# Kernel tuning notes

Hardware: AMD Instinct MI355X
Metric: run time of the kernel (lower is better)

Reference implementation:

```python
import jax, jax.numpy as jnp
import numpy as np

B, NC, NL, E, H = 64, 32, 64, 256, 256
CCLIP = 10.0


def _norm(x):
    # eps avoids NaN grads when two sampled nodes coincide
    return jnp.sqrt(jnp.sum(x * x, axis=-1) + 1e-12)


def setup_inputs() -> dict:
    key = jax.random.key(0)
    ks = jax.random.split(key, 24)
    s = 0.05
    inp = {
        "node_context": jax.random.normal(ks[0], (B, NC, NL, E), jnp.float32),
        "cell_context": jax.random.normal(ks[1], (B, NC, E), jnp.float32),
        "original_data": jax.random.uniform(ks[2], (B, NC, NL, 2), jnp.float32),
        "high_mask": jnp.zeros((B, NC), jnp.int32),
        "low_mask": jnp.zeros((B, NC, NL), jnp.int32),
        # high decoder params
        "init_w": jax.random.uniform(ks[3], (2 * E,), jnp.float32, -1.0, 1.0),
        "Wc": jax.random.normal(ks[4], (E, E), jnp.float32) * s,
        "bc": jnp.zeros((E,), jnp.float32),
        "Wv": jax.random.normal(ks[5], (2 * E, E), jnp.float32) * s,
        "bv": jnp.zeros((E,), jnp.float32),
        "hWq": jax.random.normal(ks[6], (E, H), jnp.float32) * s,
        "hbq": jnp.zeros((H,), jnp.float32),
        "hWr": jax.random.normal(ks[7], (E, H), jnp.float32) * s,
        "hbr": jnp.zeros((H,), jnp.float32),
        "hv": jax.random.normal(ks[8], (H,), jnp.float32) * s,
        # low decoder params
        "low_init_w": jax.random.uniform(ks[9], (2 * E,), jnp.float32, -1.0, 1.0),
        "lWc": jax.random.normal(ks[10], (E, E), jnp.float32) * s,
        "lbc": jnp.zeros((E,), jnp.float32),
        "lWv": jax.random.normal(ks[11], (2 * E, E), jnp.float32) * s,
        "lbv": jnp.zeros((E,), jnp.float32),
        "lWq": jax.random.normal(ks[12], (E, H), jnp.float32) * s,
        "lbq": jnp.zeros((H,), jnp.float32),
        "lWr": jax.random.normal(ks[13], (E, H), jnp.float32) * s,
        "lbr": jnp.zeros((H,), jnp.float32),
        "lv": jax.random.normal(ks[14], (H,), jnp.float32) * s,
    }
    return inp


def reference(node_context, cell_context, original_data, high_mask, low_mask,
              init_w, Wc, bc, Wv, bv, hWq, hbq, hWr, hbr, hv,
              low_init_w, lWc, lbc, lWv, lbv, lWq, lbq, lWr, lbr, lv):
    B_, NC_, NL_, E_ = node_context.shape
    aB = jnp.arange(B_)

    def pointer_logits(query, target, mask, Wq, bq, Wr, br, v):
        # query [B,E], target [B,S,E], mask [B,S] (1 = visited/blocked)
        q = query @ Wq + bq                                  # [B,H]
        r = jnp.einsum('bse,eh->bsh', target, Wr) + br       # [B,S,H]
        u = jnp.tanh(q[:, None, :] + r) @ v                  # [B,S]
        u = CCLIP * jnp.tanh(u)
        return jnp.where(mask > 0, -1e9, u)

    def low_decode(ctx, coords, mask, key):
        # ctx [B,NL,E], coords [B,NL,2], mask [B,NL]
        h_bar = jnp.mean(ctx, axis=1) @ lWc + lbc
        query = h_bar + (low_init_w @ lWv + lbv)
        keys = jax.random.split(key, NL_)

        def sample(query, mask, k):
            logits = pointer_logits(query, ctx, mask, lWq, lbq, lWr, lbr, lv)
            idx = jax.random.categorical(k, logits)
            logp = jnp.take_along_axis(jax.nn.log_softmax(logits), idx[:, None], axis=1)[:, 0]
            return idx, logp, mask.at[aB, idx].set(1)

        idx0, logp0, mask = sample(query, mask, keys[0])
        init_h = ctx[aB, idx0]                                # first selected node embedding
        query = h_bar + (jnp.concatenate([init_h, init_h], -1) @ lWv + lbv)
        init_node = coords[:, 0]                              # tour starts at local node 0
        rew0 = _norm(coords[aB, idx0] - init_node)

        def step(carry, k):
            query, mask, cur = carry
            idx, logp, mask = sample(query, mask, k)
            h = ctx[aB, idx]
            query = h_bar + (jnp.concatenate([init_h, h], -1) @ lWv + lbv)
            rew = _norm(coords[aB, idx] - coords[aB, cur])
            return (query, mask, idx), (logp, rew)

        (_, _, last_idx), (logps, rews) = jax.lax.scan(step, (query, mask, idx0), keys[1:])
        return logp0 + logps.sum(0), rew0 + rews.sum(0), init_node, coords[aB, last_idx]

    h_bar = jnp.mean(cell_context, axis=1) @ Wc + bc
    query = h_bar + (init_w @ Wv + bv)
    hkeys = jax.random.split(jax.random.key(42), NC_)
    lkeys = jax.random.split(jax.random.key(7), NC_)

    def sample_high(query, hmask, k):
        logits = pointer_logits(query, cell_context, hmask, hWq, hbq, hWr, hbr, hv)
        idx = jax.random.categorical(k, logits)
        logp = jnp.take_along_axis(jax.nn.log_softmax(logits), idx[:, None], axis=1)[:, 0]
        return idx, logp, hmask.at[aB, idx].set(1)

    def run_cell(idx, k_lo, last_node):
        llogp, lR, init_node, new_last = low_decode(
            node_context[aB, idx], original_data[aB, idx], low_mask[aB, idx], k_lo)
        return llogp, lR + _norm(init_node - last_node), new_last

    # high step 0 (sets init_h)
    idx0, hlogp0, hmask = sample_high(query, high_mask, hkeys[0])
    init_h = cell_context[aB, idx0]
    query = h_bar + (jnp.concatenate([init_h, init_h], -1) @ Wv + bv)
    llogp0, rew0, last_node = run_cell(idx0, lkeys[0], jnp.zeros((B_, 2), node_context.dtype))

    def high_step(carry, ks):
        query, hmask, last_node = carry
        k_hi, k_lo = ks
        idx, hlogp, hmask = sample_high(query, hmask, k_hi)
        h = cell_context[aB, idx]
        query = h_bar + (jnp.concatenate([init_h, h], -1) @ Wv + bv)
        llogp, rew, last_node = run_cell(idx, k_lo, last_node)
        return (query, hmask, last_node), (hlogp + llogp, rew)

    _, (logps, rews) = jax.lax.scan(high_step, (query, hmask, last_node), (hkeys[1:], lkeys[1:]))
    total_log_prob = hlogp0 + llogp0 + logps.sum(0)   # [B]
    total_reward = rew0 + rews.sum(0)                 # [B]
    return total_log_prob, total_reward
```

## Files before the change

kernel.cpp:

```cpp
#include <hip/hip_runtime.h>
#include <cstdint>
#include <cstddef>

#define B_  64
#define NC_ 32
#define NL_ 64
#define E_  256
#define H_  256

__device__ __forceinline__ void tf2x32(unsigned k0, unsigned k1,
                                       unsigned c0, unsigned c1,
                                       unsigned &o0, unsigned &o1) {
  unsigned ks2 = k0 ^ k1 ^ 0x1BD11BDAu;
  unsigned x0 = c0 + k0, x1 = c1 + k1;
#define TFR(r) { x0 += x1; x1 = (x1 << r) | (x1 >> (32 - r)); x1 ^= x0; }
  TFR(13) TFR(15) TFR(26) TFR(6)   x0 += k1;  x1 += ks2 + 1u;
  TFR(17) TFR(29) TFR(16) TFR(24)  x0 += ks2; x1 += k0 + 2u;
  TFR(13) TFR(15) TFR(26) TFR(6)   x0 += k0;  x1 += k1 + 3u;
  TFR(17) TFR(29) TFR(16) TFR(24)  x0 += k1;  x1 += ks2 + 4u;
  TFR(13) TFR(15) TFR(26) TFR(6)   x0 += ks2; x1 += k0 + 5u;
#undef TFR
  o0 = x0; o1 = x1;
}

__device__ __forceinline__ float gumbel_bits(unsigned k0, unsigned k1, unsigned flat) {
  unsigned a, b;
  tf2x32(k0, k1, 0u, flat, a, b);
  unsigned bits = a ^ b;
  float f = __uint_as_float(0x3F800000u | (bits >> 9)) - 1.0f;
  f = fmaxf(f, 1.17549435e-38f);
  return -logf(-logf(f));
}

__device__ __forceinline__ float ftanh(float x) {
  float e = __expf(2.0f * x);
  return fmaf(-2.0f, __builtin_amdgcn_rcpf(e + 1.0f), 1.0f);
}

__global__ __launch_bounds__(256) void k0_kernel(
    const float* __restrict__ init_w, const float* __restrict__ Wv,
    const float* __restrict__ hWq,
    const float* __restrict__ low_init_w, const float* __restrict__ lWv,
    const float* __restrict__ lWq, const float* __restrict__ lvin,
    unsigned* __restrict__ hkeys, unsigned* __restrict__ lkeys,
    float* __restrict__ g0h, float* __restrict__ g0l,
    float* __restrict__ Lsum) {
  int tid = threadIdx.x;
  __shared__ float s_iwv[E_], s_liwv[E_];
  if (tid < 32) {
    unsigned a, b;
    tf2x32(0u, 42u, 0u, (unsigned)tid, a, b);
    hkeys[2*tid] = a; hkeys[2*tid+1] = b;
    tf2x32(0u, 7u, 0u, (unsigned)tid, a, b);
    lkeys[2*tid] = a; lkeys[2*tid+1] = b;
  }
  if (tid == 0) {
    float s = 0.f;
    for (int k = 0; k < 256; ++k) s += lvin[k];
    Lsum[0] = s;
  }
  {
    float a = 0.f, a2 = 0.f;
    for (int k = 0; k < 2*E_; ++k) {
      a  = fmaf(init_w[k],     Wv[(size_t)k*E_ + tid], a);
      a2 = fmaf(low_init_w[k], lWv[(size_t)k*E_ + tid], a2);
    }
    s_iwv[tid] = a; s_liwv[tid] = a2;
  }
  __syncthreads();
  {
    float a = 0.f, a2 = 0.f;
    for (int e = 0; e < E_; ++e) {
      a  = fmaf(s_iwv[e],  hWq[(size_t)e*H_ + tid], a);
      a2 = fmaf(s_liwv[e], lWq[(size_t)e*H_ + tid], a2);
    }
    g0h[tid] = a; g0l[tid] = a2;
  }
}

__global__ __launch_bounds__(256) void k_mean(const float* __restrict__ in,
                                              float* __restrict__ out, int G) {
  int row = blockIdx.x, h = threadIdx.x;
  const float* p = in + (size_t)row * G * E_ + h;
  float a = 0.f;
  for (int g = 0; g < G; ++g) a += p[(size_t)g * E_];
  out[(size_t)row * E_ + h] = a * (1.0f / G);
}

__global__ __launch_bounds__(256) void k_gemm(
    const float* __restrict__ A, int lda, const float* __restrict__ avec,
    const float* __restrict__ W, const float* __restrict__ bias,
    float* __restrict__ C, int M, int N, int K) {
  __shared__ float As[16][17];
  int i0 = blockIdx.x * 16, j0 = blockIdx.y * 64;
  int tx = threadIdx.x & 63, ty = threadIdx.x >> 6;
  int j = j0 + tx;
  float acc[4] = {0.f, 0.f, 0.f, 0.f};
  for (int kk = 0; kk < K; kk += 16) {
    int r = threadIdx.x >> 4, cc = threadIdx.x & 15;
    float av = A[(size_t)(i0 + r) * lda + kk + cc];
    if (avec) av += avec[kk + cc];
    As[r][cc] = av;
    __syncthreads();
#pragma unroll
    for (int kt = 0; kt < 16; ++kt) {
      float w = W[(size_t)(kk + kt) * N + j];
#pragma unroll
      for (int k2 = 0; k2 < 4; ++k2)
        acc[k2] = fmaf(As[ty*4 + k2][kt], w, acc[k2]);
    }
    __syncthreads();
  }
  float bb = bias ? bias[j] : 0.f;
#pragma unroll
  for (int k2 = 0; k2 < 4; ++k2)
    C[(size_t)(i0 + ty*4 + k2) * N + j] = acc[k2] + bb;
}

__global__ __launch_bounds__(256) void k_gemmg(
    const float* __restrict__ nodectx, const int* __restrict__ arow,
    const int* __restrict__ cellarr, const float* __restrict__ W,
    const float* __restrict__ hq0l, float* __restrict__ C) {
  __shared__ float As[16][17];
  __shared__ int rows[16];
  int i0 = blockIdx.x * 16, j0 = blockIdx.y * 64;
  int tx = threadIdx.x & 63, ty = threadIdx.x >> 6;
  int j = j0 + tx;
  if (threadIdx.x < 16) rows[threadIdx.x] = arow[i0 + threadIdx.x];
  __syncthreads();
  float acc[4] = {0.f, 0.f, 0.f, 0.f};
  for (int kk = 0; kk < 256; kk += 16) {
    int r = threadIdx.x >> 4, cc = threadIdx.x & 15;
    As[r][cc] = nodectx[(size_t)rows[r] * 256 + kk + cc];
    __syncthreads();
#pragma unroll
    for (int kt = 0; kt < 16; ++kt) {
      float w = W[(size_t)(kk + kt) * 256 + j];
#pragma unroll
      for (int k2 = 0; k2 < 4; ++k2)
        acc[k2] = fmaf(As[ty*4 + k2][kt], w, acc[k2]);
    }
    __syncthreads();
  }
#pragma unroll
  for (int k2 = 0; k2 < 4; ++k2) {
    int row = i0 + ty*4 + k2;
    C[(size_t)row * 256 + j] = acc[k2] + hq0l[(size_t)cellarr[row] * 256 + j];
  }
}

__global__ __launch_bounds__(256, 2) void k_bgemm(
    const float* __restrict__ A, const float* __restrict__ Wr,
    const float* __restrict__ Alm, const float* __restrict__ lbr,
    float* __restrict__ Rout, float* __restrict__ Qout) {
  __shared__ float As[16][132];
  __shared__ float Ws[16][132];
  int bx = blockIdx.x, by = blockIdx.y;
  const float* Wbase = (by < 2) ? Wr : Alm;
  float* Cbase = (by < 2) ? Rout : Qout;
  int jb = (by & 1) * 128;
  bool doBias = (by < 2);
  int m0 = bx * 128;
  int tid = threadIdx.x;
  int tx = tid & 15, ty = tid >> 4;
  float acc[8][8];
#pragma unroll
  for (int i = 0; i < 8; ++i)
#pragma unroll
    for (int j = 0; j < 8; ++j) acc[i][j] = 0.f;

  for (int kc = 0; kc < 256; kc += 16) {
    {
      int kq = (tid & 3) * 4;
#pragma unroll
      for (int p = 0; p < 2; ++p) {
        int m = (tid >> 2) + p * 64;
        float4 a4 = *(const float4*)&A[(size_t)(m0 + m) * 256 + kc + kq];
        As[kq + 0][m] = a4.x; As[kq + 1][m] = a4.y;
        As[kq + 2][m] = a4.z; As[kq + 3][m] = a4.w;
      }
      int k = tid >> 4;
      int c4 = (tid & 15) * 8;
      float4 w0 = *(const float4*)&Wbase[(size_t)(kc + k) * 256 + jb + c4];
      float4 w1 = *(const float4*)&Wbase[(size_t)(kc + k) * 256 + jb + c4 + 4];
      *(float4*)&Ws[k][c4] = w0;
      *(float4*)&Ws[k][c4 + 4] = w1;
    }
    __syncthreads();
#pragma unroll
    for (int k = 0; k < 16; ++k) {
      float4 a0 = *(float4*)&As[k][ty * 8];
      float4 a1 = *(float4*)&As[k][ty * 8 + 4];
      float4 w0 = *(float4*)&Ws[k][tx * 8];
      float4 w1 = *(float4*)&Ws[k][tx * 8 + 4];
      float av[8] = {a0.x, a0.y, a0.z, a0.w, a1.x, a1.y, a1.z, a1.w};
      float wv[8] = {w0.x, w0.y, w0.z, w0.w, w1.x, w1.y, w1.z, w1.w};
#pragma unroll
      for (int i = 0; i < 8; ++i)
#pragma unroll
        for (int j = 0; j < 8; ++j)
          acc[i][j] = fmaf(av[i], wv[j], acc[i][j]);
    }
    __syncthreads();
  }
  float bias[8];
#pragma unroll
  for (int j = 0; j < 8; ++j)
    bias[j] = doBias ? lbr[jb + tx * 8 + j] : 0.f;
#pragma unroll
  for (int i = 0; i < 8; ++i) {
    float4 o0 = make_float4(acc[i][0] + bias[0], acc[i][1] + bias[1],
                            acc[i][2] + bias[2], acc[i][3] + bias[3]);
    float4 o1 = make_float4(acc[i][4] + bias[4], acc[i][5] + bias[5],
                            acc[i][6] + bias[6], acc[i][7] + bias[7]);
    size_t base = (size_t)(m0 + ty * 8 + i) * 256 + jb + tx * 8;
    *(float4*)&Cbase[base] = o0;
    *(float4*)&Cbase[base + 4] = o1;
  }
}

__global__ __launch_bounds__(256) void k_u0k(
    const float* __restrict__ R, const float* __restrict__ hq0l,
    const float* __restrict__ g0l, const float* __restrict__ lv,
    float* __restrict__ u0) {
  int cell = blockIdx.x, tid = threadIdx.x, lane = tid & 63, w = tid >> 6;
  __shared__ float qs[256];
  qs[tid] = hq0l[(size_t)cell*256 + tid] + g0l[tid];
  __syncthreads();
  float lvr[4], qsr[4];
#pragma unroll
  for (int q = 0; q < 4; ++q) { lvr[q] = lv[lane + 64*q]; qsr[q] = qs[lane + 64*q]; }
  const float* Rb = R + (size_t)cell * 16384;
  for (int i = 0; i < 16; ++i) {
    int n = w*16 + i;
    const float* rr = Rb + (size_t)n*256;
    float a = 0.f;
#pragma unroll
    for (int q = 0; q < 4; ++q)
      a = fmaf(lvr[q], ftanh(qsr[q] + rr[lane + 64*q]), a);
#pragma unroll
    for (int off = 32; off; off >>= 1) a += __shfl_xor(a, off);
    if (lane == 0) u0[(size_t)cell*64 + n] = 10.0f * ftanh(a);
  }
}

__global__ __launch_bounds__(256) void k_high(
    const float* __restrict__ cell_ctx, const int* __restrict__ high_mask,
    const float* __restrict__ hv,
    const float* __restrict__ ws_hq0h, const float* __restrict__ ws_g0h,
    const float* __restrict__ ws_Qh, const float* __restrict__ ws_rhigh,
    const float* __restrict__ ws_M1h, const unsigned* __restrict__ ws_hkeys,
    int* __restrict__ ws_hidx, float* __restrict__ ws_hlogp) {
  int b = blockIdx.x, tid = threadIdx.x;
  int lane = tid & 63, w = tid >> 6;
  __shared__ float s[H_], addM[H_], hq0[H_], g0[H_], hvv[H_];
  __shared__ float uarr[NC_];
  __shared__ int prev_s;
  __shared__ unsigned hm_s;
  __shared__ float acc_s;
  hq0[tid] = ws_hq0h[(size_t)b*H_ + tid];
  g0[tid] = ws_g0h[tid];
  hvv[tid] = hv[tid];
  if (tid == 0) {
    unsigned m = 0;
    for (int c = 0; c < NC_; ++c) if (high_mask[b*NC_ + c] > 0) m |= (1u << c);
    hm_s = m; acc_s = 0.f; prev_s = 0;
  }
  __syncthreads();
  for (int t = 0; t < NC_; ++t) {
    {
      float v = hq0[tid];
      if (t == 0) v += g0[tid];
      else        v += addM[tid] + ws_Qh[(size_t)(b*NC_ + prev_s)*H_ + tid];
      s[tid] = v;
    }
    __syncthreads();
    unsigned hm = hm_s;
    for (int q8 = 0; q8 < 8; ++q8) {
      int cidx = w*8 + q8;
      if ((hm >> cidx) & 1u) continue;
      const float* rr = ws_rhigh + (size_t)(b*NC_ + cidx)*H_;
      float a = 0.f;
#pragma unroll
      for (int jj = 0; jj < 4; ++jj) {
        int h = lane + 64*jj;
        a += hvv[h] * ftanh(s[h] + rr[h]);
      }
#pragma unroll
      for (int off = 32; off; off >>= 1) a += __shfl_xor(a, off);
      if (lane == 0) uarr[cidx] = 10.0f * ftanh(a);
    }
    __syncthreads();
    if (w == 0) {
      int cidx = lane;
      bool valid = (cidx < NC_);
      bool masked = valid && ((hm >> cidx) & 1u);
      float logit = valid ? (masked ? -1e9f : uarr[cidx]) : -INFINITY;
      float val = -INFINITY;
      if (valid) {
        float g = gumbel_bits(ws_hkeys[2*t], ws_hkeys[2*t+1],
                              (unsigned)(b*NC_ + cidx));
        val = logit + g;
      }
      float bvv = val; int bi = valid ? cidx : 9999;
#pragma unroll
      for (int off = 32; off; off >>= 1) {
        float ov = __shfl_xor(bvv, off); int oi = __shfl_xor(bi, off);
        if (ov > bvv || (ov == bvv && oi < bi)) { bvv = ov; bi = oi; }
      }
      float m = logit;
#pragma unroll
      for (int off = 32; off; off >>= 1) m = fmaxf(m, __shfl_xor(m, off));
      float ex = (valid && !masked) ? expf(logit - m) : 0.f;
#pragma unroll
      for (int off = 32; off; off >>= 1) ex += __shfl_xor(ex, off);
      float lsel = __shfl(logit, bi);
      float logp = lsel - m - logf(ex);
      if (lane == 0) {
        acc_s += logp;
        ws_hidx[b*NC_ + t] = bi;
        hm_s = hm | (1u << bi);
        prev_s = bi;
      }
    }
    __syncthreads();
    if (t == 0) {
      {
        int idx0 = prev_s;
        const float* crow = cell_ctx + (size_t)(b*NC_ + idx0)*E_;
        float a = 0.f;
        for (int e = 0; e < E_; ++e)
          a = fmaf(crow[e], ws_M1h[(size_t)e*H_ + tid], a);
        addM[tid] = a;
      }
      __syncthreads();
    }
  }
  if (tid == 0) ws_hlogp[b] = acc_s;
}

__global__ __launch_bounds__(256) void k_idx0(
    const int* __restrict__ low_mask, const unsigned* __restrict__ lkeys,
    const int* __restrict__ hidx, const float* __restrict__ u0,
    int* __restrict__ arow, int* __restrict__ cellarr) {
  int tid = threadIdx.x, lane = tid & 63, w = tid >> 6;
  int o = blockIdx.x * 4 + w;
  int b = o >> 5, t = o & 31;
  int c = hidx[o], cell = b*NC_ + c;
  float logit = (low_mask[(size_t)cell*64 + lane] > 0) ? -1e9f
               : u0[(size_t)cell*64 + lane];
  unsigned s0, s1;
  tf2x32(lkeys[2*t], lkeys[2*t+1], 0u, 0u, s0, s1);
  float g = gumbel_bits(s0, s1, (unsigned)(b*NL_ + lane));
  float val = logit + g;
  float bvv = val; int bi = lane;
#pragma unroll
  for (int off = 32; off; off >>= 1) {
    float ov = __shfl_xor(bvv, off); int oi = __shfl_xor(bi, off);
    if (ov > bvv || (ov == bvv && oi < bi)) { bvv = ov; bi = oi; }
  }
  if (lane == 0) { arow[o] = cell*64 + bi; cellarr[o] = cell; }
}

#define S_LDS 260
#define QPAD  264
__global__ __launch_bounds__(512, 6) void k_utab(
    const float* __restrict__ R, const float* __restrict__ Qm,
    const float* __restrict__ sbase, const float* __restrict__ lv,
    const float* __restrict__ Lsum, const int* __restrict__ hidx,
    float* __restrict__ U) {
  __shared__ float r_lds[32 * S_LDS];
  __shared__ float qrow[8][2 * QPAD];
  __shared__ float lvs[256];
  int tid = threadIdx.x, lane = tid & 63, w = tid >> 6;
  int o = blockIdx.x;
  int c = hidx[o], cell = (o >> 5) * NC_ + c;
  const float* Rb = R + (size_t)cell * 16384;
  const float* Qb = Qm + (size_t)cell * 16384;
  if (tid < 64) *(float4*)&lvs[4*tid] = *(const float4*)&lv[4*tid];
  float Ls = Lsum[0];
  float4 sb4 = *(const float4*)&sbase[(size_t)o*256 + 4*lane];
  int rbase = (lane >> 5) * 128;
  int nloc = lane & 31;
  float* qw = qrow[w];
  for (int p = 0; p < 2; ++p) {
    if (p) __syncthreads();
#pragma unroll
    for (int k = 0; k < 4; ++k) {
      int f = tid + 512*k;
      int nl = f >> 6, h4 = (f & 63) * 4;
      float4 v = *(const float4*)&Rb[(size_t)(p*32 + nl)*256 + h4];
      *(float4*)&r_lds[nl*S_LDS + h4] =
          make_float4(__expf(v.x + v.x), __expf(v.y + v.y),
                      __expf(v.z + v.z), __expf(v.w + v.w));
    }
    __syncthreads();
    for (int jj = 0; jj < 4; ++jj) {
      int j0 = w*8 + 2*jj;
      {
        float4 qa = *(const float4*)&Qb[(size_t)j0*256 + 4*lane];
        float4 qb = *(const float4*)&Qb[(size_t)(j0+1)*256 + 4*lane];
        *(float4*)&qw[4*lane] =
            make_float4(__expf(2.f*(sb4.x + qa.x)), __expf(2.f*(sb4.y + qa.y)),
                        __expf(2.f*(sb4.z + qa.z)), __expf(2.f*(sb4.w + qa.w)));
        *(float4*)&qw[QPAD + 4*lane] =
            make_float4(__expf(2.f*(sb4.x + qb.x)), __expf(2.f*(sb4.y + qb.y)),
                        __expf(2.f*(sb4.z + qb.z)), __expf(2.f*(sb4.w + qb.w)));
      }
      float4 acc0 = make_float4(0.f, 0.f, 0.f, 0.f);
      float4 acc1 = make_float4(0.f, 0.f, 0.f, 0.f);
#pragma unroll 8
      for (int cc = 0; cc < 32; ++cc) {
        int hh = rbase + 4*cc;
        float4 rv = *(float4*)&r_lds[nloc*S_LDS + hh];
        float4 l4 = *(float4*)&lvs[hh];
        float4 q0 = *(float4*)&qw[hh];
        float4 q1 = *(float4*)&qw[QPAD + hh];
        acc0.x = fmaf(l4.x, __builtin_amdgcn_rcpf(fmaf(q0.x, rv.x, 1.f)), acc0.x);
        acc0.y = fmaf(l4.y, __builtin_amdgcn_rcpf(fmaf(q0.y, rv.y, 1.f)), acc0.y);
        acc0.z = fmaf(l4.z, __builtin_amdgcn_rcpf(fmaf(q0.z, rv.z, 1.f)), acc0.z);
        acc0.w = fmaf(l4.w, __builtin_amdgcn_rcpf(fmaf(q0.w, rv.w, 1.f)), acc0.w);
        acc1.x = fmaf(l4.x, __builtin_amdgcn_rcpf(fmaf(q1.x, rv.x, 1.f)), acc1.x);
        acc1.y = fmaf(l4.y, __builtin_amdgcn_rcpf(fmaf(q1.y, rv.y, 1.f)), acc1.y);
        acc1.z = fmaf(l4.z, __builtin_amdgcn_rcpf(fmaf(q1.z, rv.z, 1.f)), acc1.z);
        acc1.w = fmaf(l4.w, __builtin_amdgcn_rcpf(fmaf(q1.w, rv.w, 1.f)), acc1.w);
      }
      float a0 = (acc0.x + acc0.y) + (acc0.z + acc0.w);
      float a1 = (acc1.x + acc1.y) + (acc1.z + acc1.w);
      a0 += __shfl_xor(a0, 32);
      a1 += __shfl_xor(a1, 32);
      if (lane < 32) {
        float* Uo = U + (size_t)o*4096 + j0*64 + p*32 + lane;
        Uo[0]  = 10.0f * ftanh(fmaf(-2.f, a0, Ls));
        Uo[64] = 10.0f * ftanh(fmaf(-2.f, a1, Ls));
      }
    }
  }
}

__global__ __launch_bounds__(256) void k_lowseq(
    const float* __restrict__ orig, const int* __restrict__ low_mask,
    const unsigned* __restrict__ lkeys, const int* __restrict__ hidx,
    const float* __restrict__ u0, const float* __restrict__ U,
    float* __restrict__ llogp, float* __restrict__ lRr,
    float* __restrict__ lastn, float* __restrict__ initn) {
  int tid = threadIdx.x, lane = tid & 63, w = tid >> 6;
  int o = blockIdx.x * 4 + w;
  int b = o >> 5, t = o & 31;
  int c = hidx[o], cell = b*NC_ + c;
  float cx = orig[(size_t)cell*128 + 2*lane];
  float cy = orig[(size_t)cell*128 + 2*lane + 1];
  int maskb = (low_mask[(size_t)cell*64 + lane] > 0) ? 1 : 0;
  unsigned sk0, sk1;
  tf2x32(lkeys[2*t], lkeys[2*t+1], 0u, (unsigned)lane, sk0, sk1);
  float row = u0[(size_t)cell*64 + lane];
  float px = __shfl(cx, 0), py = __shfl(cy, 0);
  float ix = px, iy = py;
  float lp = 0.f, rw = 0.f;
  const float* Ub = U + (size_t)o * 4096;
  for (int s = 0; s < NL_; ++s) {
    float logit = maskb ? -1e9f : row;
    unsigned k0 = (unsigned)__shfl((int)sk0, s);
    unsigned k1 = (unsigned)__shfl((int)sk1, s);
    float g = gumbel_bits(k0, k1, (unsigned)(b*NL_ + lane));
    float val = logit + g;
    float bvv = val; int bi = lane;
#pragma unroll
    for (int off = 32; off; off >>= 1) {
      float ov = __shfl_xor(bvv, off); int oi = __shfl_xor(bi, off);
      if (ov > bvv || (ov == bvv && oi < bi)) { bvv = ov; bi = oi; }
    }
    float nrow = Ub[(size_t)bi*64 + lane];
    float m = logit;
#pragma unroll
    for (int off = 32; off; off >>= 1) m = fmaxf(m, __shfl_xor(m, off));
    float ex = maskb ? 0.f : expf(logit - m);
#pragma unroll
    for (int off = 32; off; off >>= 1) ex += __shfl_xor(ex, off);
    float lsel = __shfl(logit, bi);
    lp += lsel - m - logf(ex);
    float bx = __shfl(cx, bi), by = __shfl(cy, bi);
    float dx = bx - px, dy = by - py;
    rw += sqrtf(dx*dx + dy*dy + 1e-12f);
    px = bx; py = by;
    if (lane == bi) maskb = 1;
    row = nrow;
  }
  if (lane == 0) {
    llogp[o] = lp; lRr[o] = rw;
    lastn[2*o] = px; lastn[2*o+1] = py;
    initn[2*o] = ix; initn[2*o+1] = iy;
  }
}

__global__ __launch_bounds__(64) void k_stitch(
    const float* __restrict__ ws_hlogp, const float* __restrict__ ws_llogp,
    const float* __restrict__ ws_lR, const float* __restrict__ ws_lastn,
    const float* __restrict__ ws_initn, float* __restrict__ out) {
  int b = threadIdx.x;
  if (b >= B_) return;
  float lp = ws_hlogp[b], rw = 0.f, lx = 0.f, ly = 0.f;
  for (int t = 0; t < NC_; ++t) {
    int o = b*NC_ + t;
    lp += ws_llogp[o];
    float dx = ws_initn[2*o] - lx, dy = ws_initn[2*o+1] - ly;
    rw += ws_lR[o] + sqrtf(dx*dx + dy*dy + 1e-12f);
    lx = ws_lastn[2*o]; ly = ws_lastn[2*o+1];
  }
  out[b] = lp;
  out[B_ + b] = rw;
}

extern "C" void kernel_launch(void* const* d_in, const int* in_sizes, int n_in,
                              void* d_out, int out_size, void* d_ws, size_t ws_size,
                              hipStream_t stream) {
  const float* node_ctx  = (const float*)d_in[0];
  const float* cell_ctx  = (const float*)d_in[1];
  const float* orig      = (const float*)d_in[2];
  const int*   high_mask = (const int*)d_in[3];
  const int*   low_mask  = (const int*)d_in[4];
  const float* init_w    = (const float*)d_in[5];
  const float* Wc        = (const float*)d_in[6];
  const float* bc        = (const float*)d_in[7];
  const float* Wv        = (const float*)d_in[8];
  const float* bv        = (const float*)d_in[9];
  const float* hWq       = (const float*)d_in[10];
  const float* hbq       = (const float*)d_in[11];
  const float* hWr       = (const float*)d_in[12];
  const float* hbr       = (const float*)d_in[13];
  const float* hv        = (const float*)d_in[14];
  const float* low_init_w= (const float*)d_in[15];
  const float* lWc       = (const float*)d_in[16];
  const float* lbc       = (const float*)d_in[17];
  const float* lWv       = (const float*)d_in[18];
  const float* lbv       = (const float*)d_in[19];
  const float* lWq       = (const float*)d_in[20];
  const float* lbq       = (const float*)d_in[21];
  const float* lWr       = (const float*)d_in[22];
  const float* lbr       = (const float*)d_in[23];
  const float* lv        = (const float*)d_in[24];
  float* out = (float*)d_out;

  char* ws = (char*)d_ws;
  size_t off = 0;
  auto alloc = [&](size_t bytes) -> void* {
    void* p = ws + off;
    off += (bytes + 255) & ~(size_t)255;
    return p;
  };
  unsigned* w_hkeys = (unsigned*)alloc(32*2*4);
  unsigned* w_lkeys = (unsigned*)alloc(32*2*4);
  int*   w_hidx  = (int*)alloc(2048*4);
  int*   w_arow  = (int*)alloc(2048*4);
  int*   w_cell  = (int*)alloc(2048*4);
  float* w_hlogp = (float*)alloc(64*4);
  float* w_llogp = (float*)alloc(2048*4);
  float* w_lR    = (float*)alloc(2048*4);
  float* w_lastn = (float*)alloc(2048*2*4);
  float* w_initn = (float*)alloc(2048*2*4);
  float* w_g0h   = (float*)alloc(256*4);
  float* w_g0l   = (float*)alloc(256*4);
  float* w_Lsum  = (float*)alloc(4);
  float* w_M1h   = (float*)alloc((size_t)65536*4);
  float* w_Ah    = (float*)alloc((size_t)65536*4);
  float* w_M1l   = (float*)alloc((size_t)65536*4);
  float* w_Al    = (float*)alloc((size_t)65536*4);
  float* w_mcc   = (float*)alloc((size_t)64*256*4);
  float* w_mnc   = (float*)alloc((size_t)2048*256*4);
  float* w_hbh   = (float*)alloc((size_t)64*256*4);
  float* w_hq0h  = (float*)alloc((size_t)64*256*4);
  float* w_rhigh = (float*)alloc((size_t)2048*256*4);
  float* w_Qh    = (float*)alloc((size_t)2048*256*4);
  float* w_hbl   = (float*)alloc((size_t)2048*256*4);
  float* w_hq0l  = (float*)alloc((size_t)2048*256*4);
  float* w_u0    = (float*)alloc((size_t)2048*64*4);
  float* w_sbase = (float*)alloc((size_t)2048*256*4);
  float* w_U     = (float*)alloc((size_t)2048*4096*4);
  float* w_R     = (float*)alloc((size_t)2048*64*256*4);
  float* w_Qm    = (float*)alloc((size_t)2048*64*256*4);
  (void)ws_size; (void)in_sizes; (void)n_in; (void)out_size;

  k0_kernel<<<1, 256, 0, stream>>>(init_w, Wv, hWq, low_init_w, lWv, lWq, lv,
                                   w_hkeys, w_lkeys, w_g0h, w_g0l, w_Lsum);
  k_mean<<<2048, 256, 0, stream>>>(node_ctx, w_mnc, 64);
  k_mean<<<64, 256, 0, stream>>>(cell_ctx, w_mcc, 32);

  dim3 g256(16, 4), g2048(128, 4), g64(4, 4);
  k_gemm<<<g256, 256, 0, stream>>>(Wv,            256, nullptr, hWq, nullptr, w_M1h, 256, 256, 256);
  k_gemm<<<g256, 256, 0, stream>>>(Wv + 65536,    256, nullptr, hWq, nullptr, w_Ah,  256, 256, 256);
  k_gemm<<<g256, 256, 0, stream>>>(lWv,           256, nullptr, lWq, nullptr, w_M1l, 256, 256, 256);
  k_gemm<<<g256, 256, 0, stream>>>(lWv + 65536,   256, nullptr, lWq, nullptr, w_Al,  256, 256, 256);
  k_gemm<<<g2048, 256, 0, stream>>>(cell_ctx, 256, nullptr, hWr, hbr, w_rhigh, 2048, 256, 256);
  k_gemm<<<g2048, 256, 0, stream>>>(cell_ctx, 256, nullptr, w_Ah, nullptr, w_Qh, 2048, 256, 256);
  k_gemm<<<g64,   256, 0, stream>>>(w_mcc, 256, nullptr, Wc,  bc,  w_hbh, 64,   256, 256);
  k_gemm<<<g2048, 256, 0, stream>>>(w_mnc, 256, nullptr, lWc, lbc, w_hbl, 2048, 256, 256);
  k_gemm<<<g64,   256, 0, stream>>>(w_hbh, 256, bv,  hWq, hbq, w_hq0h, 64,   256, 256);
  k_gemm<<<g2048, 256, 0, stream>>>(w_hbl, 256, lbv, lWq, lbq, w_hq0l, 2048, 256, 256);

  k_bgemm<<<dim3(1024, 4), 256, 0, stream>>>(node_ctx, lWr, w_Al, lbr, w_R, w_Qm);
  k_u0k<<<2048, 256, 0, stream>>>(w_R, w_hq0l, w_g0l, lv, w_u0);

  k_high<<<64, 256, 0, stream>>>(cell_ctx, high_mask, hv, w_hq0h, w_g0h, w_Qh,
                                 w_rhigh, w_M1h, w_hkeys, w_hidx, w_hlogp);
  k_idx0<<<512, 256, 0, stream>>>(low_mask, w_lkeys, w_hidx, w_u0, w_arow, w_cell);
  k_gemmg<<<dim3(128, 4), 256, 0, stream>>>(node_ctx, w_arow, w_cell, w_M1l,
                                            w_hq0l, w_sbase);
  k_utab<<<2048, 512, 0, stream>>>(w_R, w_Qm, w_sbase, lv, w_Lsum, w_hidx, w_U);
  k_lowseq<<<512, 256, 0, stream>>>(orig, low_mask, w_lkeys, w_hidx, w_u0, w_U,
                                    w_llogp, w_lR, w_lastn, w_initn);
  k_stitch<<<1, 64, 0, stream>>>(w_hlogp, w_llogp, w_lR, w_lastn, w_initn, out);
}
```

Measured before the change: 1.417 ms.

## Double-buffer k_bgemm shared tiles with register prefetch and reorder grid

Switches the batched GEMM over node contexts to double-buffered shared-memory tiles, prefetching the next K-slice into registers while the current slice is computed. This leaves one barrier per iteration instead of two. The grid is transposed so the four column/weight blocks that share an A tile launch back to back, which should improve L2 reuse of node_ctx. The W shared-memory read pattern changes to strided float4 halves to reduce bank conflicts, and the occupancy hint rises to 3 blocks, which risks register spills and doubles shared memory per block.

New measurement: 2.087 ms. 47.3% more time.

```diff
diff --git a/kernel.cpp b/kernel.cpp
--- a/kernel.cpp
+++ b/kernel.cpp
@@ -149,73 +149,93 @@
   }
 }
 
-__global__ __launch_bounds__(256, 2) void k_bgemm(
+__global__ __launch_bounds__(256, 3) void k_bgemm(
     const float* __restrict__ A, const float* __restrict__ Wr,
     const float* __restrict__ Alm, const float* __restrict__ lbr,
     float* __restrict__ Rout, float* __restrict__ Qout) {
-  __shared__ float As[16][132];
-  __shared__ float Ws[16][132];
-  int bx = blockIdx.x, by = blockIdx.y;
+  __shared__ float As[2][16][132];
+  __shared__ float Ws[2][16][132];
+  int by = blockIdx.x;
+  int m0 = blockIdx.y * 128;
   const float* Wbase = (by < 2) ? Wr : Alm;
   float* Cbase = (by < 2) ? Rout : Qout;
   int jb = (by & 1) * 128;
   bool doBias = (by < 2);
-  int m0 = bx * 128;
   int tid = threadIdx.x;
   int tx = tid & 15, ty = tid >> 4;
+  int kq = (tid & 3) * 4, ma = tid >> 2;
+  int kw = tid >> 4, c4 = (tid & 15) * 8;
+
   float acc[8][8];
 #pragma unroll
   for (int i = 0; i < 8; ++i)
 #pragma unroll
     for (int j = 0; j < 8; ++j) acc[i][j] = 0.f;
 
+  float4 a0, a1, w0, w1;
+  a0 = *(const float4*)&A[(size_t)(m0 + ma) * 256 + kq];
+  a1 = *(const float4*)&A[(size_t)(m0 + ma + 64) * 256 + kq];
+  w0 = *(const float4*)&Wbase[(size_t)kw * 256 + jb + c4];
+  w1 = *(const float4*)&Wbase[(size_t)kw * 256 + jb + c4 + 4];
+  As[0][kq+0][ma] = a0.x; As[0][kq+1][ma] = a0.y;
+  As[0][kq+2][ma] = a0.z; As[0][kq+3][ma] = a0.w;
+  As[0][kq+0][ma+64] = a1.x; As[0][kq+1][ma+64] = a1.y;
+  As[0][kq+2][ma+64] = a1.z; As[0][kq+3][ma+64] = a1.w;
+  *(float4*)&Ws[0][kw][c4]     = w0;
+  *(float4*)&Ws[0][kw][c4 + 4] = w1;
+  __syncthreads();
+
   for (int kc = 0; kc < 256; kc += 16) {
-    {
-      int kq = (tid & 3) * 4;
-#pragma unroll
-      for (int p = 0; p < 2; ++p) {
-        int m = (tid >> 2) + p * 64;
-        float4 a4 = *(const float4*)&A[(size_t)(m0 + m) * 256 + kc + kq];
-        As[kq + 0][m] = a4.x; As[kq + 1][m] = a4.y;
-        As[kq + 2][m] = a4.z; As[kq + 3][m] = a4.w;
-      }
-      int k = tid >> 4;
-      int c4 = (tid & 15) * 8;
-      float4 w0 = *(const float4*)&Wbase[(size_t)(kc + k) * 256 + jb + c4];
-      float4 w1 = *(const float4*)&Wbase[(size_t)(kc + k) * 256 + jb + c4 + 4];
-      *(float4*)&Ws[k][c4] = w0;
-      *(float4*)&Ws[k][c4 + 4] = w1;
-    }
-    __syncthreads();
+    int cur = (kc >> 4) & 1;
+    bool more = (kc + 16) < 256;
+    if (more) {
+      a0 = *(const float4*)&A[(size_t)(m0 + ma) * 256 + kc + 16 + kq];
+      a1 = *(const float4*)&A[(size_t)(m0 + ma + 64) * 256 + kc + 16 + kq];
+      w0 = *(const float4*)&Wbase[(size_t)(kc + 16 + kw) * 256 + jb + c4];
+      w1 = *(const float4*)&Wbase[(size_t)(kc + 16 + kw) * 256 + jb + c4 + 4];
+    }
+    const float (*Asb)[132] = As[cur];
+    const float (*Wsb)[132] = Ws[cur];
 #pragma unroll
     for (int k = 0; k < 16; ++k) {
-      float4 a0 = *(float4*)&As[k][ty * 8];
-      float4 a1 = *(float4*)&As[k][ty * 8 + 4];
-      float4 w0 = *(float4*)&Ws[k][tx * 8];
-      float4 w1 = *(float4*)&Ws[k][tx * 8 + 4];
-      float av[8] = {a0.x, a0.y, a0.z, a0.w, a1.x, a1.y, a1.z, a1.w};
-      float wv[8] = {w0.x, w0.y, w0.z, w0.w, w1.x, w1.y, w1.z, w1.w};
+      float4 va0 = *(const float4*)&Asb[k][ty * 8];
+      float4 va1 = *(const float4*)&Asb[k][ty * 8 + 4];
+      float4 vw0 = *(const float4*)&Wsb[k][tx * 4];
+      float4 vw1 = *(const float4*)&Wsb[k][tx * 4 + 64];
+      float av[8] = {va0.x, va0.y, va0.z, va0.w, va1.x, va1.y, va1.z, va1.w};
+      float wv[8] = {vw0.x, vw0.y, vw0.z, vw0.w, vw1.x, vw1.y, vw1.z, vw1.w};
 #pragma unroll
       for (int i = 0; i < 8; ++i)
 #pragma unroll
         for (int j = 0; j < 8; ++j)
           acc[i][j] = fmaf(av[i], wv[j], acc[i][j]);
     }
-    __syncthreads();
-  }
-  float bias[8];
-#pragma unroll
-  for (int j = 0; j < 8; ++j)
-    bias[j] = doBias ? lbr[jb + tx * 8 + j] : 0.f;
+    if (more) {
+      int nb = cur ^ 1;
+      As[nb][kq+0][ma] = a0.x; As[nb][kq+1][ma] = a0.y;
+      As[nb][kq+2][ma] = a0.z; As[nb][kq+3][ma] = a0.w;
+      As[nb][kq+0][ma+64] = a1.x; As[nb][kq+1][ma+64] = a1.y;
+      As[nb][kq+2][ma+64] = a1.z; As[nb][kq+3][ma+64] = a1.w;
+      *(float4*)&Ws[nb][kw][c4]     = w0;
+      *(float4*)&Ws[nb][kw][c4 + 4] = w1;
+      __syncthreads();
+    }
+  }
+  float bias0[4], bias1[4];
+#pragma unroll
+  for (int j = 0; j < 4; ++j) {
+    bias0[j] = doBias ? lbr[jb + tx * 4 + j] : 0.f;
+    bias1[j] = doBias ? lbr[jb + 64 + tx * 4 + j] : 0.f;
+  }
 #pragma unroll
   for (int i = 0; i < 8; ++i) {
-    float4 o0 = make_float4(acc[i][0] + bias[0], acc[i][1] + bias[1],
-                            acc[i][2] + bias[2], acc[i][3] + bias[3]);
-    float4 o1 = make_float4(acc[i][4] + bias[4], acc[i][5] + bias[5],
-                            acc[i][6] + bias[6], acc[i][7] + bias[7]);
-    size_t base = (size_t)(m0 + ty * 8 + i) * 256 + jb + tx * 8;
-    *(float4*)&Cbase[base] = o0;
-    *(float4*)&Cbase[base + 4] = o1;
+    float4 o0 = make_float4(acc[i][0] + bias0[0], acc[i][1] + bias0[1],
+                            acc[i][2] + bias0[2], acc[i][3] + bias0[3]);
+    float4 o1 = make_float4(acc[i][4] + bias1[0], acc[i][5] + bias1[1],
+                            acc[i][6] + bias1[2], acc[i][7] + bias1[3]);
+    size_t row = (size_t)(m0 + ty * 8 + i);
+    *(float4*)&Cbase[row * 256 + jb + tx * 4] = o0;
+    *(float4*)&Cbase[row * 256 + jb + 64 + tx * 4] = o1;
   }
 }
 
@@ -597,7 +617,7 @@
   k_gemm<<<g64,   256, 0, stream>>>(w_hbh, 256, bv,  hWq, hbq, w_hq0h, 64,   256, 256);
   k_gemm<<<g2048, 256, 0, stream>>>(w_hbl, 256, lbv, lWq, lbq, w_hq0l, 2048, 256, 256);
 
-  k_bgemm<<<dim3(1024, 4), 256, 0, stream>>>(node_ctx, lWr, w_Al, lbr, w_R, w_Qm);
+  k_bgemm<<<dim3(4, 1024), 256, 0, stream>>>(node_ctx, lWr, w_Al, lbr, w_R, w_Qm);
   k_u0k<<<2048, 256, 0, stream>>>(w_R, w_hq0l, w_g0l, lv, w_u0);
 
   k_high<<<64, 256, 0, stream>>>(cell_ctx, high_mask, hv, w_hq0h, w_g0h, w_Qh,
```
